# Performance work log

Measured on AMD Instinct MI355X. Metric: run time of the kernel, lower is better.

## Reference

```python
import jax, jax.numpy as jnp
import numpy as np

B, D, S = 8, 128, 4096

def setup_inputs() -> dict:
    key = jax.random.key(0)
    ks = jax.random.split(key, 7)
    sd = 1.0 / np.sqrt(D)
    return {
        "x": jax.random.normal(ks[0], (B, D, S), dtype=jnp.float32),
        "Wq": jax.random.normal(ks[1], (D, D), dtype=jnp.float32) * sd,
        "bq": jax.random.normal(ks[2], (D,), dtype=jnp.float32) * sd,
        "Wk": jax.random.normal(ks[3], (D, D), dtype=jnp.float32) * sd,
        "bk": jax.random.normal(ks[4], (D,), dtype=jnp.float32) * sd,
        "Wv": jax.random.normal(ks[5], (D, D), dtype=jnp.float32) * sd,
        "bv": jax.random.normal(ks[6], (D,), dtype=jnp.float32) * sd,
    }

def reference(x, Wq, bq, Wk, bk, Wv, bv):
    # x: (B, D, S) -> (B, S, D)
    xt = jnp.transpose(x, (0, 2, 1))
    scale = jnp.asarray(D, xt.dtype) ** 0.5
    # torch Linear: y = x @ W.T + b
    Q = jnp.einsum('bsd,ed->bse', xt, Wq) + bq
    K = jnp.einsum('bsd,ed->bse', xt, Wk) + bk
    V = jnp.einsum('bsd,ed->bse', xt, Wv) + bv
    scores = jnp.einsum('bqd,bkd->bqk', Q, K) / scale  # (B, S, S)
    attn = jax.nn.softmax(scores, axis=-1)
    attended = jnp.einsum('bqk,bkd->bqd', attn, V)
    out = xt + attended  # residual
    return jnp.transpose(out, (0, 2, 1))  # back to (B, D, S)
```

## Files before the change

### kernel.cpp

```cpp
#include <hip/hip_runtime.h>
#include <hip/hip_bf16.h>

#define B_ 8
#define D_ 128
#define S_ 4096

typedef short short8 __attribute__((ext_vector_type(8)));
typedef float f32x4  __attribute__((ext_vector_type(4)));
typedef float f32x16 __attribute__((ext_vector_type(16)));
typedef unsigned int uint;
typedef uint uint4v __attribute__((ext_vector_type(4)));

#define EXP2F(x) exp2f(x)

__device__ __forceinline__ short f2bf(float f) {
    __hip_bfloat16 h = __float2bfloat16(f);
    return *reinterpret_cast<short*>(&h);
}

__device__ __forceinline__ uint cvtpk(float lo, float hi) {
    uint r;
    asm("v_cvt_pk_bf16_f32 %0, %1, %2" : "=v"(r) : "v"(lo), "v"(hi));
    return r;
}

__device__ __forceinline__ void gload16(const void* g, void* l) {
    __builtin_amdgcn_global_load_lds(
        (const __attribute__((address_space(1))) void*)g,
        (__attribute__((address_space(3))) void*)l, 16, 0, 0);
}

__device__ __forceinline__ float max3f(float a, float b, float c) {
    return fmaxf(fmaxf(a, b), c);
}

__global__ __launch_bounds__(256) void wpack_kernel(
    const float* __restrict__ Wq, const float* __restrict__ Wk,
    const float* __restrict__ Wv, short* __restrict__ Wf)
{
    int g = blockIdx.x * 256 + threadIdx.x;
    int lane = g & 63, kc = (g >> 6) & 3, n = (g >> 8) & 7, wm = g >> 11;
    const float* W = (wm == 0) ? Wq : (wm == 1) ? Wk : Wv;
    int row = n * 16 + (lane & 15);
    int col = kc * 32 + (lane >> 4) * 8;
    short8 o;
    #pragma unroll
    for (int j = 0; j < 8; ++j) o[j] = f2bf(W[row * 128 + col + j]);
    *((short8*)Wf + g) = o;
}

__global__ __launch_bounds__(256) void qkv_kernel(
    const float* __restrict__ x, const short* __restrict__ Wf,
    const float* __restrict__ bq, const float* __restrict__ bk,
    const float* __restrict__ bv,
    short* __restrict__ Qo, short* __restrict__ Ko, short* __restrict__ Vo)
{
    __shared__ float xt[64 * 132];
    const int b  = blockIdx.y;
    const int s0 = blockIdx.x * 64;
    const int t  = threadIdx.x;
    const int w    = t >> 6;
    const int lane = t & 63;
    const int lr   = lane & 15;
    const int lg   = lane >> 4;

    const float* xb = x + (size_t)b * D_ * S_;
    #pragma unroll
    for (int it = 0; it < 32; ++it) {
        int d = it * 4 + (t >> 6);
        int s = t & 63;
        xt[s * 132 + d] = xb[(size_t)d * S_ + s0 + s];
    }
    __syncthreads();

    short8 xtf[4];
    {
        const float* base = &xt[(w * 16 + lr) * 132 + lg * 8];
        #pragma unroll
        for (int kc = 0; kc < 4; ++kc) {
            float4 a = *(const float4*)(base + kc * 32);
            float4 c = *(const float4*)(base + kc * 32 + 4);
            short8 f;
            f[0] = f2bf(a.x); f[1] = f2bf(a.y); f[2] = f2bf(a.z); f[3] = f2bf(a.w);
            f[4] = f2bf(c.x); f[5] = f2bf(c.y); f[6] = f2bf(c.z); f[7] = f2bf(c.w);
            xtf[kc] = f;
        }
    }

    const float qs = 0.08838834764831845f * 1.4426950408889634f;
    const short8* W8 = (const short8*)Wf;
    const size_t bSD = (size_t)b * S_ * D_;
    const size_t bDS = (size_t)b * D_ * S_;

    #pragma unroll
    for (int n = 0; n < 8; ++n) {
        f32x4 aq = (f32x4){0.f, 0.f, 0.f, 0.f};
        f32x4 ak = (f32x4){0.f, 0.f, 0.f, 0.f};
        f32x4 av = (f32x4){0.f, 0.f, 0.f, 0.f};
        #pragma unroll
        for (int kc = 0; kc < 4; ++kc) {
            short8 wq = W8[(      n * 4 + kc) * 64 + lane];
            short8 wk = W8[(32  + n * 4 + kc) * 64 + lane];
            short8 wv = W8[(64  + n * 4 + kc) * 64 + lane];
            aq = __builtin_amdgcn_mfma_f32_16x16x32_bf16(xtf[kc], wq, aq, 0, 0, 0);
            ak = __builtin_amdgcn_mfma_f32_16x16x32_bf16(xtf[kc], wk, ak, 0, 0, 0);
            av = __builtin_amdgcn_mfma_f32_16x16x32_bf16(wv, xtf[kc], av, 0, 0, 0);
        }
        int e = n * 16 + lr;
        float bqe = bq[e], bke = bk[e];
        #pragma unroll
        for (int r = 0; r < 4; ++r) {
            size_t off = (bSD + (size_t)(s0 + w * 16 + lg * 4 + r) * D_) + e;
            Qo[off] = f2bf((aq[r] + bqe) * qs);
            Ko[off] = f2bf(ak[r] + bke);
        }
        #pragma unroll
        for (int r = 0; r < 4; ++r) {
            int ev = n * 16 + lg * 4 + r;
            Vo[bDS + (size_t)ev * S_ + s0 + w * 16 + lr] = f2bf(av[r] + bv[ev]);
        }
    }
}

__global__ __launch_bounds__(512, 2) void attn_kernel(
    const short* __restrict__ Q, const short* __restrict__ K,
    const short* __restrict__ Vt, const float* __restrict__ x,
    float* __restrict__ out)
{
    extern __shared__ __align__(16) char smem[];
    const int lin = blockIdx.x;
    const int b   = lin & 7;
    const int q0  = (lin >> 3) * 128;
    const int tid  = threadIdx.x;
    const int w    = tid >> 6;
    const int lane = tid & 63;
    const int q    = lane & 31;
    const int hi   = lane >> 5;
    const int half = w >> 2;
    const int ww   = w & 3;

    const size_t bSD = (size_t)b * S_ * D_;

    short8 qf[8];
    {
        const short* Qrow = Q + bSD + (size_t)(q0 + ww * 32 + q) * D_ + hi * 8;
        #pragma unroll
        for (int c = 0; c < 8; ++c)
            qf[c] = *(const short8*)(Qrow + c * 16);
    }

    f32x16 o[4];
    #pragma unroll
    for (int dt = 0; dt < 4; ++dt)
        #pragma unroll
        for (int i = 0; i < 16; ++i) o[dt][i] = 0.f;
    float m = -1e30f, lsum = 0.f;

    const short* Kb = K + bSD;
    const short* Vb = Vt + (size_t)b * D_ * S_;
    const int ktbase = half * 32;

    auto KH = [&](int t) -> const char* {
        return smem + ((t & 1) * 2 + half) * 16384;
    };
    auto VH = [&](int t) -> const char* {
        return smem + 65536 + ((t % 3) * 2 + half) * 16384;
    };

    auto stage = [&](int kt) {
        const short* Kg = Kb + (size_t)(ktbase + kt) * 64 * D_;
        const short* Vg = Vb + (size_t)(ktbase + kt) * 64;
        char* Kd = smem + ((kt & 1) * 2 + half) * 16384;
        char* Vd = smem + 65536 + ((kt % 3) * 2 + half) * 16384;
        #pragma unroll
        for (int i = 0; i < 4; ++i) {
            int ki = ww * 4 + i;
            int r  = ki * 4 + (lane >> 4);
            gload16(Kg + r * D_ + (((lane & 15) ^ (r & 7)) * 8), Kd + ki * 1024);
        }
        #pragma unroll
        for (int i = 0; i < 4; ++i) {
            int vi = ww * 4 + i;
            int r  = vi * 8 + (lane >> 3);
            gload16(Vg + (size_t)r * S_ + (((lane & 7) ^ (lane >> 3)) * 8),
                    Vd + vi * 1024);
        }
    };

    auto qkrun = [&](const char* Kh, f32x16& acc0, f32x16& acc1) {
        #pragma unroll
        for (int i = 0; i < 16; ++i) { acc0[i] = 0.f; acc1[i] = 0.f; }
        short8 kf[3][2];
        {
            int co0 = ((0 + hi) ^ (q & 7)) * 16;
            int co1 = ((2 + hi) ^ (q & 7)) * 16;
            kf[0][0] = *(const short8*)(Kh + q * 256 + co0);
            kf[0][1] = *(const short8*)(Kh + (32 + q) * 256 + co0);
            kf[1][0] = *(const short8*)(Kh + q * 256 + co1);
            kf[1][1] = *(const short8*)(Kh + (32 + q) * 256 + co1);
        }
        __builtin_amdgcn_s_setprio(1);
        #pragma unroll
        for (int c = 0; c < 8; ++c) {
            if (c < 6) {
                int co = (((c + 2) * 2 + hi) ^ (q & 7)) * 16;
                kf[(c + 2) % 3][0] = *(const short8*)(Kh + q * 256 + co);
                kf[(c + 2) % 3][1] = *(const short8*)(Kh + (32 + q) * 256 + co);
            }
            acc0 = __builtin_amdgcn_mfma_f32_32x32x16_bf16(kf[c % 3][0], qf[c], acc0, 0, 0, 0);
            acc1 = __builtin_amdgcn_mfma_f32_32x32x16_bf16(kf[c % 3][1], qf[c], acc1, 0, 0, 0);
        }
        __builtin_amdgcn_s_setprio(0);
    };

    auto finish = [&](f32x16& acc0, f32x16& acc1, const char* Vh) {
        float a0 = max3f(acc0[0],  acc0[1],  acc0[2]);
        float a1 = max3f(acc0[3],  acc0[4],  acc0[5]);
        float a2 = max3f(acc0[6],  acc0[7],  acc0[8]);
        float a3 = max3f(acc0[9],  acc0[10], acc0[11]);
        float a4 = max3f(acc0[12], acc0[13], acc0[14]);
        float a5 = max3f(acc1[0],  acc1[1],  acc1[2]);
        float a6 = max3f(acc1[3],  acc1[4],  acc1[5]);
        float a7 = max3f(acc1[6],  acc1[7],  acc1[8]);
        float a8 = max3f(acc1[9],  acc1[10], acc1[11]);
        float a9 = max3f(acc1[12], acc1[13], acc1[14]);
        float b0 = max3f(a0, a1, a2);
        float b1 = max3f(a3, a4, acc0[15]);
        float b2 = max3f(a5, a6, a7);
        float b3 = max3f(a8, a9, acc1[15]);
        float tm = fmaxf(max3f(b0, b1, b2), b3);
        tm = fmaxf(tm, __shfl_xor(tm, 32));
        if (!__all(tm <= m + 8.f)) {
            float mn   = fmaxf(m, tm);
            float corr = EXP2F(m - mn);
            m = mn; lsum *= corr;
            #pragma unroll
            for (int dt = 0; dt < 4; ++dt)
                #pragma unroll
                for (int r = 0; r < 16; ++r) o[dt][r] *= corr;
        }
        #pragma unroll
        for (int r = 0; r < 16; ++r) acc0[r] = EXP2F(acc0[r] - m);
        #pragma unroll
        for (int r = 0; r < 16; ++r) acc1[r] = EXP2F(acc1[r] - m);

        short8 pf[4];
        #pragma unroll
        for (int kc = 0; kc < 4; ++kc) {
            const f32x16& a = (kc < 2) ? acc0 : acc1;
            int c1 = (kc & 1) * 8;
            uint W0 = cvtpk(a[c1 + 0], a[c1 + 1]);
            uint W1 = cvtpk(a[c1 + 2], a[c1 + 3]);
            uint W2 = cvtpk(a[c1 + 4], a[c1 + 5]);
            uint W3 = cvtpk(a[c1 + 6], a[c1 + 7]);
            asm("v_permlane32_swap_b32 %0, %1" : "+v"(W0), "+v"(W2));
            asm("v_permlane32_swap_b32 %0, %1" : "+v"(W1), "+v"(W3));
            uint4v pw;
            pw.x = W0; pw.y = W1; pw.z = W2; pw.w = W3;
            pf[kc] = *reinterpret_cast<short8*>(&pw);
        }

        short8 vf[3][2];
        {
            int co0 = ((0 + hi) ^ (q & 7)) * 16;
            vf[0][0] = *(const short8*)(Vh + (0 * 32 + q) * 128 + co0);
            vf[0][1] = *(const short8*)(Vh + (1 * 32 + q) * 128 + co0);
            vf[1][0] = *(const short8*)(Vh + (2 * 32 + q) * 128 + co0);
            vf[1][1] = *(const short8*)(Vh + (3 * 32 + q) * 128 + co0);
        }
        float s0 = ((acc0[0]+acc0[1])+(acc0[2]+acc0[3]))
                 + ((acc0[4]+acc0[5])+(acc0[6]+acc0[7]));
        float s1 = ((acc0[8]+acc0[9])+(acc0[10]+acc0[11]))
                 + ((acc0[12]+acc0[13])+(acc0[14]+acc0[15]));
        float s2 = ((acc1[0]+acc1[1])+(acc1[2]+acc1[3]))
                 + ((acc1[4]+acc1[5])+(acc1[6]+acc1[7]));
        float s3 = ((acc1[8]+acc1[9])+(acc1[10]+acc1[11]))
                 + ((acc1[12]+acc1[13])+(acc1[14]+acc1[15]));
        lsum += (s0 + s1) + (s2 + s3);

        __builtin_amdgcn_s_setprio(1);
        #pragma unroll
        for (int s = 0; s < 8; ++s) {
            if (s < 6) {
                int i0 = 2 * s + 4, i1 = 2 * s + 5;
                int coA = (((i0 >> 2) * 2 + hi) ^ (q & 7)) * 16;
                int coB = (((i1 >> 2) * 2 + hi) ^ (q & 7)) * 16;
                vf[(s + 2) % 3][0] = *(const short8*)(Vh + ((i0 & 3) * 32 + q) * 128 + coA);
                vf[(s + 2) % 3][1] = *(const short8*)(Vh + ((i1 & 3) * 32 + q) * 128 + coB);
            }
            o[(2 * s) & 3] = __builtin_amdgcn_mfma_f32_32x32x16_bf16(
                vf[s % 3][0], pf[(2 * s) >> 2], o[(2 * s) & 3], 0, 0, 0);
            o[(2 * s + 1) & 3] = __builtin_amdgcn_mfma_f32_32x32x16_bf16(
                vf[s % 3][1], pf[(2 * s + 1) >> 2], o[(2 * s + 1) & 3], 0, 0, 0);
        }
        __builtin_amdgcn_s_setprio(0);
    };

    f32x16 acc0, acc1;

    stage(0);
    __syncthreads();

    if (half == 0) {
        for (int t = 0; t < 32; ++t) {
            if (t < 31) stage(t + 1);
            qkrun(KH(t), acc0, acc1);
            finish(acc0, acc1, VH(t));
            __syncthreads();
        }
    } else {
        stage(1);
        qkrun(KH(0), acc0, acc1);
        __syncthreads();
        for (int t = 1; t < 32; ++t) {
            if (t < 31) stage(t + 1);
            finish(acc0, acc1, VH(t - 1));
            qkrun(KH(t), acc0, acc1);
            __syncthreads();
        }
        finish(acc0, acc1, VH(31));
    }

    lsum += __shfl_xor(lsum, 32);

    if (half == 1) {
        float* obuf = (float*)(smem + ww * 16384);
        #pragma unroll
        for (int dt = 0; dt < 4; ++dt)
            #pragma unroll
            for (int r = 0; r < 16; ++r) {
                int dl = dt * 32 + (r & 3) + 8 * (r >> 2) + 4 * hi;
                obuf[dl * 32 + q] = o[dt][r];
            }
        if (hi == 0) {
            float* ml = (float*)(smem + 65536 + ww * 256);
            ml[q * 2]     = m;
            ml[q * 2 + 1] = lsum;
        }
    }
    __syncthreads();
    if (half == 0) {
        const float* obuf = (const float*)(smem + ww * 16384);
        const float* ml   = (const float*)(smem + 65536 + ww * 256);
        float m2 = ml[q * 2], l2 = ml[q * 2 + 1];
        float M  = fmaxf(m, m2);
        float c1 = EXP2F(m - M), c2 = EXP2F(m2 - M);
        float inv = 1.0f / (lsum * c1 + l2 * c2);
        const float* xb = x   + (size_t)b * D_ * S_;
        float*       ob = out + (size_t)b * D_ * S_;
        int s = q0 + ww * 32 + q;
        #pragma unroll
        for (int dt = 0; dt < 4; ++dt)
            #pragma unroll
            for (int r = 0; r < 16; ++r) {
                int dl = dt * 32 + (r & 3) + 8 * (r >> 2) + 4 * hi;
                float val = (o[dt][r] * c1 + obuf[dl * 32 + q] * c2) * inv;
                size_t g = (size_t)dl * S_ + s;
                ob[g] = xb[g] + val;
            }
    }
}

extern "C" void kernel_launch(void* const* d_in, const int* in_sizes, int n_in,
                              void* d_out, int out_size, void* d_ws, size_t ws_size,
                              hipStream_t stream) {
    const float* x  = (const float*)d_in[0];
    const float* Wq = (const float*)d_in[1];
    const float* bq = (const float*)d_in[2];
    const float* Wk = (const float*)d_in[3];
    const float* bk = (const float*)d_in[4];
    const float* Wv = (const float*)d_in[5];
    const float* bv = (const float*)d_in[6];
    float* out = (float*)d_out;

    size_t n = (size_t)B_ * S_ * D_;
    short* Qw = (short*)d_ws;
    short* Kw = Qw + n;
    short* Vw = Kw + n;
    short* Wf = (short*)d_out;

    wpack_kernel<<<24, 256, 0, stream>>>(Wq, Wk, Wv, Wf);

    dim3 grid(S_ / 64, B_);
    qkv_kernel<<<grid, 256, 0, stream>>>(x, Wf, bq, bk, bv, Qw, Kw, Vw);

    int smemB = 163840;
    (void)hipFuncSetAttribute((const void*)attn_kernel,
                              hipFuncAttributeMaxDynamicSharedMemorySize, smemB);
    attn_kernel<<<256, 512, smemB, stream>>>(Qw, Kw, Vw, x, out);
}
```

Measured before the change: 121.8 us.

## Software-pipeline QK of next tile with softmax and PV of current tile

Restructures the attention main loop so both halves run the same ping-pong schedule. The QK^T MFMAs for tile t+1 are issued while tile t's exp/pack and PV run, with sched_group_barrier hints to interleave MFMA, LDS reads and VALU work. The shared-memory buffers are reassigned so K is triple-buffered and V double-buffered, and K staging runs two tiles ahead. This is meant to hide softmax VALU latency behind matrix ops, at the cost of two extra live accumulator sets and more register pressure.

Result: slower. 127.8 us (+4.9%).

```diff
diff --git a/kernel.cpp b/kernel.cpp
--- a/kernel.cpp
+++ b/kernel.cpp
@@ -161,23 +161,25 @@
     const int ktbase = half * 32;
 
     auto KH = [&](int t) -> const char* {
-        return smem + ((t & 1) * 2 + half) * 16384;
+        return smem + ((t % 3) * 2 + half) * 16384;
     };
     auto VH = [&](int t) -> const char* {
-        return smem + 65536 + ((t % 3) * 2 + half) * 16384;
-    };
-
-    auto stage = [&](int kt) {
+        return smem + 98304 + ((t & 1) * 2 + half) * 16384;
+    };
+
+    auto stageK = [&](int kt) {
         const short* Kg = Kb + (size_t)(ktbase + kt) * 64 * D_;
-        const short* Vg = Vb + (size_t)(ktbase + kt) * 64;
-        char* Kd = smem + ((kt & 1) * 2 + half) * 16384;
-        char* Vd = smem + 65536 + ((kt % 3) * 2 + half) * 16384;
+        char* Kd = smem + ((kt % 3) * 2 + half) * 16384;
         #pragma unroll
         for (int i = 0; i < 4; ++i) {
             int ki = ww * 4 + i;
             int r  = ki * 4 + (lane >> 4);
             gload16(Kg + r * D_ + (((lane & 15) ^ (r & 7)) * 8), Kd + ki * 1024);
         }
+    };
+    auto stageV = [&](int kt) {
+        const short* Vg = Vb + (size_t)(ktbase + kt) * 64;
+        char* Vd = smem + 98304 + ((kt & 1) * 2 + half) * 16384;
         #pragma unroll
         for (int i = 0; i < 4; ++i) {
             int vi = ww * 4 + i;
@@ -187,9 +189,9 @@
         }
     };
 
-    auto qkrun = [&](const char* Kh, f32x16& acc0, f32x16& acc1) {
-        #pragma unroll
-        for (int i = 0; i < 16; ++i) { acc0[i] = 0.f; acc1[i] = 0.f; }
+    auto qkrun = [&](const char* Kh, f32x16& A0, f32x16& A1) {
+        #pragma unroll
+        for (int i = 0; i < 16; ++i) { A0[i] = 0.f; A1[i] = 0.f; }
         short8 kf[3][2];
         {
             int co0 = ((0 + hi) ^ (q & 7)) * 16;
@@ -199,7 +201,6 @@
             kf[1][0] = *(const short8*)(Kh + q * 256 + co1);
             kf[1][1] = *(const short8*)(Kh + (32 + q) * 256 + co1);
         }
-        __builtin_amdgcn_s_setprio(1);
         #pragma unroll
         for (int c = 0; c < 8; ++c) {
             if (c < 6) {
@@ -207,27 +208,26 @@
                 kf[(c + 2) % 3][0] = *(const short8*)(Kh + q * 256 + co);
                 kf[(c + 2) % 3][1] = *(const short8*)(Kh + (32 + q) * 256 + co);
             }
-            acc0 = __builtin_amdgcn_mfma_f32_32x32x16_bf16(kf[c % 3][0], qf[c], acc0, 0, 0, 0);
-            acc1 = __builtin_amdgcn_mfma_f32_32x32x16_bf16(kf[c % 3][1], qf[c], acc1, 0, 0, 0);
-        }
-        __builtin_amdgcn_s_setprio(0);
-    };
-
-    auto finish = [&](f32x16& acc0, f32x16& acc1, const char* Vh) {
-        float a0 = max3f(acc0[0],  acc0[1],  acc0[2]);
-        float a1 = max3f(acc0[3],  acc0[4],  acc0[5]);
-        float a2 = max3f(acc0[6],  acc0[7],  acc0[8]);
-        float a3 = max3f(acc0[9],  acc0[10], acc0[11]);
-        float a4 = max3f(acc0[12], acc0[13], acc0[14]);
-        float a5 = max3f(acc1[0],  acc1[1],  acc1[2]);
-        float a6 = max3f(acc1[3],  acc1[4],  acc1[5]);
-        float a7 = max3f(acc1[6],  acc1[7],  acc1[8]);
-        float a8 = max3f(acc1[9],  acc1[10], acc1[11]);
-        float a9 = max3f(acc1[12], acc1[13], acc1[14]);
+            A0 = __builtin_amdgcn_mfma_f32_32x32x16_bf16(kf[c % 3][0], qf[c], A0, 0, 0, 0);
+            A1 = __builtin_amdgcn_mfma_f32_32x32x16_bf16(kf[c % 3][1], qf[c], A1, 0, 0, 0);
+        }
+    };
+
+    auto part1 = [&](const f32x16& A0, const f32x16& A1) {
+        float a0 = max3f(A0[0],  A0[1],  A0[2]);
+        float a1 = max3f(A0[3],  A0[4],  A0[5]);
+        float a2 = max3f(A0[6],  A0[7],  A0[8]);
+        float a3 = max3f(A0[9],  A0[10], A0[11]);
+        float a4 = max3f(A0[12], A0[13], A0[14]);
+        float a5 = max3f(A1[0],  A1[1],  A1[2]);
+        float a6 = max3f(A1[3],  A1[4],  A1[5]);
+        float a7 = max3f(A1[6],  A1[7],  A1[8]);
+        float a8 = max3f(A1[9],  A1[10], A1[11]);
+        float a9 = max3f(A1[12], A1[13], A1[14]);
         float b0 = max3f(a0, a1, a2);
-        float b1 = max3f(a3, a4, acc0[15]);
+        float b1 = max3f(a3, a4, A0[15]);
         float b2 = max3f(a5, a6, a7);
-        float b3 = max3f(a8, a9, acc1[15]);
+        float b3 = max3f(a8, a9, A1[15]);
         float tm = fmaxf(max3f(b0, b1, b2), b3);
         tm = fmaxf(tm, __shfl_xor(tm, 32));
         if (!__all(tm <= m + 8.f)) {
@@ -239,15 +239,16 @@
                 #pragma unroll
                 for (int r = 0; r < 16; ++r) o[dt][r] *= corr;
         }
-        #pragma unroll
-        for (int r = 0; r < 16; ++r) acc0[r] = EXP2F(acc0[r] - m);
-        #pragma unroll
-        for (int r = 0; r < 16; ++r) acc1[r] = EXP2F(acc1[r] - m);
-
-        short8 pf[4];
+    };
+
+    auto exppack = [&](f32x16& A0, f32x16& A1, short8* pf) {
+        #pragma unroll
+        for (int r = 0; r < 16; ++r) A0[r] = EXP2F(A0[r] - m);
+        #pragma unroll
+        for (int r = 0; r < 16; ++r) A1[r] = EXP2F(A1[r] - m);
         #pragma unroll
         for (int kc = 0; kc < 4; ++kc) {
-            const f32x16& a = (kc < 2) ? acc0 : acc1;
+            const f32x16& a = (kc < 2) ? A0 : A1;
             int c1 = (kc & 1) * 8;
             uint W0 = cvtpk(a[c1 + 0], a[c1 + 1]);
             uint W1 = cvtpk(a[c1 + 2], a[c1 + 3]);
@@ -259,7 +260,19 @@
             pw.x = W0; pw.y = W1; pw.z = W2; pw.w = W3;
             pf[kc] = *reinterpret_cast<short8*>(&pw);
         }
-
+    };
+
+    auto sgb = [&]() {
+        #pragma unroll
+        for (int s8 = 0; s8 < 8; ++s8) {
+            __builtin_amdgcn_sched_group_barrier(0x100, 2, 0);
+            __builtin_amdgcn_sched_group_barrier(0x008, 2, 0);
+            __builtin_amdgcn_sched_group_barrier(0x002, 8, 0);
+        }
+    };
+
+    auto pvrun = [&](const f32x16& A0, const f32x16& A1,
+                     const short8* pf, const char* Vh) {
         short8 vf[3][2];
         {
             int co0 = ((0 + hi) ^ (q & 7)) * 16;
@@ -268,14 +281,10 @@
             vf[1][0] = *(const short8*)(Vh + (2 * 32 + q) * 128 + co0);
             vf[1][1] = *(const short8*)(Vh + (3 * 32 + q) * 128 + co0);
         }
-        float s0 = ((acc0[0]+acc0[1])+(acc0[2]+acc0[3]))
-                 + ((acc0[4]+acc0[5])+(acc0[6]+acc0[7]));
-        float s1 = ((acc0[8]+acc0[9])+(acc0[10]+acc0[11]))
-                 + ((acc0[12]+acc0[13])+(acc0[14]+acc0[15]));
-        float s2 = ((acc1[0]+acc1[1])+(acc1[2]+acc1[3]))
-                 + ((acc1[4]+acc1[5])+(acc1[6]+acc1[7]));
-        float s3 = ((acc1[8]+acc1[9])+(acc1[10]+acc1[11]))
-                 + ((acc1[12]+acc1[13])+(acc1[14]+acc1[15]));
+        float s0 = ((A0[0]+A0[1])+(A0[2]+A0[3])) + ((A0[4]+A0[5])+(A0[6]+A0[7]));
+        float s1 = ((A0[8]+A0[9])+(A0[10]+A0[11])) + ((A0[12]+A0[13])+(A0[14]+A0[15]));
+        float s2 = ((A1[0]+A1[1])+(A1[2]+A1[3])) + ((A1[4]+A1[5])+(A1[6]+A1[7]));
+        float s3 = ((A1[8]+A1[9])+(A1[10]+A1[11])) + ((A1[12]+A1[13])+(A1[14]+A1[15]));
         lsum += (s0 + s1) + (s2 + s3);
 
         __builtin_amdgcn_s_setprio(1);
@@ -296,29 +305,49 @@
         __builtin_amdgcn_s_setprio(0);
     };
 
-    f32x16 acc0, acc1;
-
-    stage(0);
+    f32x16 aA0, aA1, aB0, aB1;
+
+    stageK(0); stageV(0); stageK(1);
     __syncthreads();
-
-    if (half == 0) {
-        for (int t = 0; t < 32; ++t) {
-            if (t < 31) stage(t + 1);
-            qkrun(KH(t), acc0, acc1);
-            finish(acc0, acc1, VH(t));
-            __syncthreads();
-        }
-    } else {
-        stage(1);
-        qkrun(KH(0), acc0, acc1);
+    qkrun(KH(0), aA0, aA1);
+
+    for (int t = 0; t < 30; t += 2) {
+        stageK(t + 2); stageV(t + 1);
+        part1(aA0, aA1);
+        {
+            short8 pf[4];
+            qkrun(KH(t + 1), aB0, aB1);
+            exppack(aA0, aA1, pf);
+            sgb();
+            pvrun(aA0, aA1, pf, VH(t));
+        }
         __syncthreads();
-        for (int t = 1; t < 32; ++t) {
-            if (t < 31) stage(t + 1);
-            finish(acc0, acc1, VH(t - 1));
-            qkrun(KH(t), acc0, acc1);
-            __syncthreads();
-        }
-        finish(acc0, acc1, VH(31));
+        stageK(t + 3); stageV(t + 2);
+        part1(aB0, aB1);
+        {
+            short8 pf[4];
+            qkrun(KH(t + 2), aA0, aA1);
+            exppack(aB0, aB1, pf);
+            sgb();
+            pvrun(aB0, aB1, pf, VH(t + 1));
+        }
+        __syncthreads();
+    }
+    stageV(31);
+    part1(aA0, aA1);
+    {
+        short8 pf[4];
+        qkrun(KH(31), aB0, aB1);
+        exppack(aA0, aA1, pf);
+        sgb();
+        pvrun(aA0, aA1, pf, VH(30));
+    }
+    __syncthreads();
+    part1(aB0, aB1);
+    {
+        short8 pf[4];
+        exppack(aB0, aB1, pf);
+        pvrun(aB0, aB1, pf, VH(31));
     }
 
     lsum += __shfl_xor(lsum, 32);
@@ -333,7 +362,7 @@
                 obuf[dl * 32 + q] = o[dt][r];
             }
         if (hi == 0) {
-            float* ml = (float*)(smem + 65536 + ww * 256);
+            float* ml = (float*)(smem + 98304 + ww * 256);
             ml[q * 2]     = m;
             ml[q * 2 + 1] = lsum;
         }
@@ -341,7 +370,7 @@
     __syncthreads();
     if (half == 0) {
         const float* obuf = (const float*)(smem + ww * 16384);
-        const float* ml   = (const float*)(smem + 65536 + ww * 256);
+        const float* ml   = (const float*)(smem + 98304 + ww * 256);
         float m2 = ml[q * 2], l2 = ml[q * 2 + 1];
         float M  = fmaxf(m, m2);
         float c1 = EXP2F(m - M), c2 = EXP2F(m2 - M);
```
